# Kernel tuning notes

Hardware: AMD Instinct MI355X
Metric: run time of the kernel (lower is better)

The kernel has to match this reference:

```python
import jax, jax.numpy as jnp
import numpy as np

N = 50000          # nodes
E = 500000         # edges (before self-loops)
G = 64             # graphs in batch
SC = 96            # scalar features
D = 32             # embedding dim
IN_DIM = SC + 5 * D  # 256
C = 128            # hidden_channels
H1 = 4             # heads in conv1
NUM_CLASSES = 5
V_OP, V_SRC, V_SINK, V_STR, V_PAY = 256, 512, 512, 128, 1024


def setup_inputs() -> dict:
    key = jax.random.key(0)
    ks = jax.random.split(key, 32)
    inp = {}
    inp['x_scalar'] = jax.random.normal(ks[0], (N, SC), jnp.float32)
    inp['x_opcode'] = jax.random.randint(ks[1], (N, 16), 0, V_OP)
    inp['x_source'] = jax.random.randint(ks[2], (N, 8), 0, V_SRC)
    inp['x_sink'] = jax.random.randint(ks[3], (N, 8), 0, V_SINK)
    inp['x_string_manip'] = jax.random.randint(ks[4], (N, 8), 0, V_STR)
    inp['x_payload'] = jax.random.randint(ks[5], (N, 8), 0, V_PAY)
    inp['edge_index'] = jax.random.randint(ks[6], (2, E), 0, N)
    # sorted graph ids with every graph non-empty
    inp['batch'] = (jnp.arange(N) * G) // N
    # learned params
    s = 0.05
    inp['emb_opcode'] = jax.random.normal(ks[7], (V_OP, D), jnp.float32)
    inp['emb_source'] = jax.random.normal(ks[8], (V_SRC, D), jnp.float32)
    inp['emb_sink'] = jax.random.normal(ks[9], (V_SINK, D), jnp.float32)
    inp['emb_string'] = jax.random.normal(ks[10], (V_STR, D), jnp.float32)
    inp['emb_payload'] = jax.random.normal(ks[11], (V_PAY, D), jnp.float32)
    inp['ln_g'] = jnp.ones((IN_DIM,), jnp.float32)
    inp['ln_b'] = jnp.zeros((IN_DIM,), jnp.float32)
    inp['W1'] = jax.random.normal(ks[12], (IN_DIM, H1 * C), jnp.float32) * s
    inp['att_src1'] = jax.random.normal(ks[13], (H1, C), jnp.float32) * s
    inp['att_dst1'] = jax.random.normal(ks[14], (H1, C), jnp.float32) * s
    inp['b1'] = jnp.zeros((H1 * C,), jnp.float32)
    inp['W2'] = jax.random.normal(ks[15], (H1 * C, C), jnp.float32) * s
    inp['att_src2'] = jax.random.normal(ks[16], (1, C), jnp.float32) * s
    inp['att_dst2'] = jax.random.normal(ks[17], (1, C), jnp.float32) * s
    inp['b2'] = jnp.zeros((C,), jnp.float32)
    inp['Wc1'] = jax.random.normal(ks[18], (C, C // 2), jnp.float32) * s
    inp['bc1'] = jnp.zeros((C // 2,), jnp.float32)
    inp['Wc2'] = jax.random.normal(ks[19], (C // 2, NUM_CLASSES), jnp.float32) * s
    inp['bc2'] = jnp.zeros((NUM_CLASSES,), jnp.float32)
    return inp


def _emb_feat(table, idx):
    # masked mean over the list dim; index 0 is padding
    e = table[idx]                                  # [N, L, D]
    mask = (idx != 0)[..., None].astype(e.dtype)    # [N, L, 1]
    return (e * mask).sum(1) / (mask.sum(1) + 1e-9)


def _layernorm(x, g, b, eps=1e-5):
    mu = x.mean(-1, keepdims=True)
    var = ((x - mu) ** 2).mean(-1, keepdims=True)
    return (x - mu) * jax.lax.rsqrt(var + eps) * g + b


def _gat_conv(x, W, att_src, att_dst, bias, src, dst, heads, out_ch, concat):
    n = x.shape[0]
    h = (x @ W).reshape(n, heads, out_ch)              # [N,H,C]
    a_src = (h * att_src).sum(-1)                      # [N,H]
    a_dst = (h * att_dst).sum(-1)                      # [N,H]
    e = jax.nn.leaky_relu(a_src[src] + a_dst[dst], 0.2)  # [E,H]
    m = jax.ops.segment_max(e, dst, num_segments=n)
    e = jnp.exp(e - m[dst])
    denom = jax.ops.segment_sum(e, dst, num_segments=n)
    alpha = e / (denom[dst] + 1e-16)                   # segment softmax over in-edges
    msg = h[src] * alpha[:, :, None]                   # [E,H,C]
    out = jax.ops.segment_sum(msg, dst, num_segments=n)  # [N,H,C]
    out = out.reshape(n, heads * out_ch) if concat else out.mean(1)
    return out + bias


def reference(x_scalar, x_opcode, x_source, x_sink, x_string_manip, x_payload,
              edge_index, batch,
              emb_opcode, emb_source, emb_sink, emb_string, emb_payload,
              ln_g, ln_b, W1, att_src1, att_dst1, b1,
              W2, att_src2, att_dst2, b2, Wc1, bc1, Wc2, bc2):
    n = x_scalar.shape[0]
    feats = jnp.concatenate([
        x_scalar,
        _emb_feat(emb_opcode, x_opcode),
        _emb_feat(emb_source, x_source),
        _emb_feat(emb_sink, x_sink),
        _emb_feat(emb_string, x_string_manip),
        _emb_feat(emb_payload, x_payload),
    ], axis=1)
    feats = _layernorm(feats, ln_g, ln_b)
    # add self loops (PyG GATConv default)
    loop = jnp.arange(n)
    src = jnp.concatenate([edge_index[0], loop])
    dst = jnp.concatenate([edge_index[1], loop])
    x = jax.nn.elu(_gat_conv(feats, W1, att_src1, att_dst1, b1, src, dst, H1, C, True))
    x = jax.nn.elu(_gat_conv(x, W2, att_src2, att_dst2, b2, src, dst, 1, C, True))
    # global max pool per graph (dropout layers are identity at inference)
    xp = jax.ops.segment_max(x, batch, num_segments=G)  # [G,C]
    hcls = jax.nn.relu(xp @ Wc1 + bc1)
    return hcls @ Wc2 + bc2
```

## Files before the change

### kernel.cpp

```cpp
#include <hip/hip_runtime.h>
#include <hip/hip_bf16.h>
#include <float.h>


#define LEAKY(e) ((e) > 0.f ? (e) : 0.2f * (e))
#define POOL_CH 32

typedef _Float16 half8 __attribute__((ext_vector_type(8)));
typedef float floatx4 __attribute__((ext_vector_type(4)));

__device__ __forceinline__ void async_copy16(const _Float16* gsrc,
                                             const _Float16* ldst) {
  __builtin_amdgcn_global_load_lds(
      (const __attribute__((address_space(1))) unsigned int*)gsrc,
      (__attribute__((address_space(3))) unsigned int*)ldst, 16, 0, 0);
}

__global__ __launch_bounds__(256) void feats_kernel(
    const float* __restrict__ xs, const int* __restrict__ xo,
    const int* __restrict__ xsrc, const int* __restrict__ xsk,
    const int* __restrict__ xst, const int* __restrict__ xp,
    const float* __restrict__ eo, const float* __restrict__ es,
    const float* __restrict__ ek, const float* __restrict__ et,
    const float* __restrict__ ep, const float* __restrict__ lng,
    const float* __restrict__ lnb, _Float16* __restrict__ feats, int n) {
  int node = blockIdx.x * 4 + (threadIdx.x >> 6);
  if (node >= n) return;
  int l = threadIdx.x & 63;

  int myidx = 0;
  if (l < 16)      myidx = xo[node * 16 + l];
  else if (l < 24) myidx = xsrc[node * 8 + (l - 16)];
  else if (l < 32) myidx = xsk[node * 8 + (l - 24)];
  else if (l < 40) myidx = xst[node * 8 + (l - 32)];
  else if (l < 48) myidx = xp[node * 8 + (l - 40)];

  const float* xrow = xs + (size_t)node * 96;
  float v0 = xrow[l];
  float v1, v2, v3;

  bool hi = (l >= 32);
  int d = l & 31;

  {
    float s = 0.f, c = 0.f;
#pragma unroll
    for (int j = 0; j < 16; j++) {
      int id = __shfl(myidx, j);
      if (hi && id != 0) { s += eo[(size_t)id * 32 + d]; c += 1.f; }
    }
    float sc = hi ? 0.f : xrow[64 + l];
    v1 = hi ? (s / (c + 1e-9f)) : sc;
  }
  {
    const float* tab = hi ? ek : es;
    int base = hi ? 24 : 16;
    float s = 0.f, c = 0.f;
#pragma unroll
    for (int j = 0; j < 8; j++) {
      int id = __shfl(myidx, base + j);
      if (id != 0) { s += tab[(size_t)id * 32 + d]; c += 1.f; }
    }
    v2 = s / (c + 1e-9f);
  }
  {
    const float* tab = hi ? ep : et;
    int base = hi ? 40 : 32;
    float s = 0.f, c = 0.f;
#pragma unroll
    for (int j = 0; j < 8; j++) {
      int id = __shfl(myidx, base + j);
      if (id != 0) { s += tab[(size_t)id * 32 + d]; c += 1.f; }
    }
    v3 = s / (c + 1e-9f);
  }

  float sum = v0 + v1 + v2 + v3;
  for (int o = 32; o; o >>= 1) sum += __shfl_xor(sum, o);
  float mu = sum * (1.f / 256.f);

  float d0 = v0 - mu, d1 = v1 - mu, d2 = v2 - mu, d3 = v3 - mu;
  float q = d0 * d0 + d1 * d1 + d2 * d2 + d3 * d3;
  for (int o = 32; o; o >>= 1) q += __shfl_xor(q, o);
  float rstd = rsqrtf(q * (1.f / 256.f) + 1e-5f);

  _Float16* frow = feats + (size_t)node * 256;
  frow[l]       = (_Float16)(d0 * rstd * lng[l] + lnb[l]);
  frow[64 + l]  = (_Float16)(d1 * rstd * lng[64 + l] + lnb[64 + l]);
  frow[128 + l] = (_Float16)(d2 * rstd * lng[128 + l] + lnb[128 + l]);
  frow[192 + l] = (_Float16)(d3 * rstd * lng[192 + l] + lnb[192 + l]);
}

__global__ __launch_bounds__(256) void transpose_both_f16(
    const float* __restrict__ W1, _Float16* __restrict__ Wt1,
    const float* __restrict__ W2, _Float16* __restrict__ Wt2) {
  int t = blockIdx.x * 256 + threadIdx.x;
  if (t < 256 * 512) {
    int n = t / 256, k = t - n * 256;
    Wt1[t] = (_Float16)W1[(size_t)k * 512 + n];
  } else {
    int u = t - 256 * 512;
    int n = u / 512, k = u - n * 512;
    Wt2[u] = (_Float16)W2[(size_t)k * 128 + n];
  }
}

__global__ __launch_bounds__(256) void gemm_f16_att(
    const _Float16* __restrict__ A, const _Float16* __restrict__ Bt,
    _Float16* __restrict__ C, const float* __restrict__ att_src,
    const float* __restrict__ att_dst, float* __restrict__ a_src_out,
    float* __restrict__ a_dst_out, int astride, int K, int N) {
  __shared__ __attribute__((aligned(16))) _Float16 As[128 * 32];
  __shared__ __attribute__((aligned(16))) _Float16 Bs[128 * 32];
  int m0 = blockIdx.y * 128;
  int n0 = blockIdx.x * 128;
  int tid = threadIdx.x;
  int wave = tid >> 6, lane = tid & 63;
  int wm = (wave >> 1) * 64, wn = (wave & 1) * 64;
  int lr = lane & 15, lq = lane >> 4;
  int wbase = tid & ~63;

  floatx4 acc[4][4] = {};

  for (int k0 = 0; k0 < K; k0 += 32) {
#pragma unroll
    for (int c = 0; c < 2; c++) {
      int sid = c * 256 + tid;
      int row = sid >> 2;
      int cs = (sid & 3) ^ (row & 3);
      const _Float16* ga = A + (size_t)(m0 + row) * K + k0 + cs * 8;
      const _Float16* gb = Bt + (size_t)(n0 + row) * K + k0 + cs * 8;
      async_copy16(ga, As + (size_t)(c * 256 + wbase) * 8);
      async_copy16(gb, Bs + (size_t)(c * 256 + wbase) * 8);
    }
    __syncthreads();

    half8 af[4], bf[4];
#pragma unroll
    for (int i = 0; i < 4; i++) {
      int row = wm + i * 16 + lr;
      af[i] = *(const half8*)(As + ((row << 2) + (lq ^ (row & 3))) * 8);
    }
#pragma unroll
    for (int j = 0; j < 4; j++) {
      int row = wn + j * 16 + lr;
      bf[j] = *(const half8*)(Bs + ((row << 2) + (lq ^ (row & 3))) * 8);
    }
#pragma unroll
    for (int i = 0; i < 4; i++)
#pragma unroll
      for (int j = 0; j < 4; j++)
        acc[i][j] =
            __builtin_amdgcn_mfma_f32_16x16x32_f16(af[i], bf[j], acc[i][j], 0, 0, 0);
    __syncthreads();
  }

#pragma unroll
  for (int i = 0; i < 4; i++) {
    int rbase = m0 + wm + i * 16 + lq * 4;
#pragma unroll
    for (int r = 0; r < 4; r++) {
      int row = rbase + r;
#pragma unroll
      for (int j = 0; j < 4; j++) {
        int col = n0 + wn + j * 16 + lr;
        C[(size_t)row * N + col] = (_Float16)acc[i][j][r];
      }
    }
  }

  float asv[4], adv[4];
#pragma unroll
  for (int j = 0; j < 4; j++) {
    int col = n0 + wn + j * 16 + lr;
    asv[j] = att_src[col];
    adv[j] = att_dst[col];
  }
  float ps[4][4], pd[4][4];
#pragma unroll
  for (int i = 0; i < 4; i++)
#pragma unroll
    for (int r = 0; r < 4; r++) {
      float s = 0.f, d = 0.f;
#pragma unroll
      for (int j = 0; j < 4; j++) {
        s += acc[i][j][r] * asv[j];
        d += acc[i][j][r] * adv[j];
      }
#pragma unroll
      for (int o = 1; o < 16; o <<= 1) {
        s += __shfl_xor(s, o);
        d += __shfl_xor(d, o);
      }
      ps[i][r] = s;
      pd[i][r] = d;
    }
  float* sred = (float*)&As[0];
  if (wn == 64 && lr == 0) {
#pragma unroll
    for (int i = 0; i < 4; i++)
#pragma unroll
      for (int r = 0; r < 4; r++) {
        int rl = wm + i * 16 + lq * 4 + r;
        sred[rl * 2] = ps[i][r];
        sred[rl * 2 + 1] = pd[i][r];
      }
  }
  __syncthreads();
  if (wn == 0 && lr == 0) {
    int hsel = n0 >> 7;
#pragma unroll
    for (int i = 0; i < 4; i++)
#pragma unroll
      for (int r = 0; r < 4; r++) {
        int rl = wm + i * 16 + lq * 4 + r;
        int row = m0 + rl;
        a_src_out[(size_t)row * astride + hsel] = ps[i][r] + sred[rl * 2];
        a_dst_out[(size_t)row * astride + hsel] = pd[i][r] + sred[rl * 2 + 1];
      }
  }
}

__global__ __launch_bounds__(256) void hist_kernel(const int* __restrict__ dst,
                                                   int* __restrict__ deg, int E) {
  int t = blockIdx.x * 256 + threadIdx.x;
  if (t < E) atomicAdd(&deg[dst[t]], 1);
}

__global__ __launch_bounds__(256) void scan_a(const int* __restrict__ deg,
                                              int* __restrict__ rowptr,
                                              int* __restrict__ bsum, int n) {
  __shared__ int sh[256];
  int b = blockIdx.x, t = threadIdx.x;
  int i = b * 256 + t;
  int v = (i < n) ? deg[i] + 1 : 0;
  sh[t] = v;
  __syncthreads();
  int x = v;
  for (int o = 1; o < 256; o <<= 1) {
    int y = (t >= o) ? sh[t - o] : 0;
    __syncthreads();
    x += y;
    sh[t] = x;
    __syncthreads();
  }
  if (i < n) rowptr[i] = x - v;
  if (t == 255) bsum[b] = x;
}

__global__ __launch_bounds__(256) void scan_c(int* __restrict__ rowptr,
                                              const int* __restrict__ bsum,
                                              int n, int total) {
  int b = blockIdx.x;
  int off = 0;
  for (int j = 0; j < b; j++) off += bsum[j];
  int i = b * 256 + threadIdx.x;
  if (i < n) rowptr[i] += off;
  else if (i == n) rowptr[n] = total;
}

__global__ __launch_bounds__(256) void fill_kernel(
    const int* __restrict__ src, const int* __restrict__ dst,
    const int* __restrict__ rowptr, int* __restrict__ cnt,
    int* __restrict__ csr_src, int E, int n) {
  int t = blockIdx.x * 256 + threadIdx.x;
  if (t < E) {
    int d = dst[t];
    int pos = rowptr[d] + atomicAdd(&cnt[d], 1);
    csr_src[pos] = src[t];
  } else if (t < E + n) {
    int i = t - E;
    csr_src[rowptr[i + 1] - 1] = i;
  }
}

__global__ __launch_bounds__(256) void gat1_agg(
    const _Float16* __restrict__ h1, const float* __restrict__ asrc,
    const float* __restrict__ adst, const int* __restrict__ rowptr,
    const int* __restrict__ csr_src, const float* __restrict__ bias,
    _Float16* __restrict__ out, int n) {
  int node = blockIdx.x * 4 + (threadIdx.x >> 6);
  if (node >= n) return;
  int l = threadIdx.x & 63;
  int hh = l >> 4;
  int li = l & 15;
  int r0 = rowptr[node];
  int deg = rowptr[node + 1] - r0;
  int cb = l * 8;

  float acc[8] = {};

  if (deg <= 64) {
    float adm = adst[node * 4 + hh];
    int s_reg[4];
    float ww[4];
    float m = -1e30f;
#pragma unroll
    for (int c = 0; c < 4; c++) {
      int k = c * 16 + li;
      int s = (k < deg) ? csr_src[r0 + k] : -1;
      s_reg[c] = s;
      float e = -1e30f;
      if (s >= 0) {
        float t = asrc[(size_t)s * 4 + hh] + adm;
        e = LEAKY(t);
      }
      ww[c] = e;
      m = fmaxf(m, e);
    }
#pragma unroll
    for (int o = 1; o < 16; o <<= 1) m = fmaxf(m, __shfl_xor(m, o));
    float sum = 0.f;
#pragma unroll
    for (int c = 0; c < 4; c++) {
      float w = (s_reg[c] >= 0) ? __expf(ww[c] - m) : 0.f;
      ww[c] = w;
      sum += w;
    }
#pragma unroll
    for (int o = 1; o < 16; o <<= 1) sum += __shfl_xor(sum, o);
    float sinv = 1.f / (sum + 1e-16f);
#pragma unroll
    for (int c = 0; c < 4; c++) ww[c] *= sinv;

#pragma unroll
    for (int c = 0; c < 4; c++) {
      int base = c * 16;
      if (base >= deg) break;
      int lim = min(16, deg - base);
      int jl = 0;
      for (; jl + 4 <= lim; jl += 4) {
        int s0 = __shfl(s_reg[c], jl);
        int s1 = __shfl(s_reg[c], jl + 1);
        int s2 = __shfl(s_reg[c], jl + 2);
        int s3 = __shfl(s_reg[c], jl + 3);
        float w0 = __shfl(ww[c], hh * 16 + jl);
        float w1 = __shfl(ww[c], hh * 16 + jl + 1);
        float w2 = __shfl(ww[c], hh * 16 + jl + 2);
        float w3 = __shfl(ww[c], hh * 16 + jl + 3);
        const half8 hv0 = *(const half8*)(h1 + (size_t)s0 * 512 + cb);
        const half8 hv1 = *(const half8*)(h1 + (size_t)s1 * 512 + cb);
        const half8 hv2 = *(const half8*)(h1 + (size_t)s2 * 512 + cb);
        const half8 hv3 = *(const half8*)(h1 + (size_t)s3 * 512 + cb);
#pragma unroll
        for (int q = 0; q < 8; q++)
          acc[q] += w0 * (float)hv0[q] + w1 * (float)hv1[q] +
                    w2 * (float)hv2[q] + w3 * (float)hv3[q];
      }
      for (; jl < lim; jl++) {
        int s0 = __shfl(s_reg[c], jl);
        float w0 = __shfl(ww[c], hh * 16 + jl);
        const half8 hv0 = *(const half8*)(h1 + (size_t)s0 * 512 + cb);
#pragma unroll
        for (int q = 0; q < 8; q++) acc[q] += w0 * (float)hv0[q];
      }
    }
  } else {
    float4 ad4 = *(const float4*)(adst + node * 4);
    float adv[4] = {ad4.x, ad4.y, ad4.z, ad4.w};
    float m[4] = {-1e30f, -1e30f, -1e30f, -1e30f};
    for (int k = l; k < deg; k += 64) {
      int s = csr_src[r0 + k];
      float4 av = *(const float4*)(asrc + (size_t)s * 4);
      float e;
      e = LEAKY(av.x + adv[0]); m[0] = fmaxf(m[0], e);
      e = LEAKY(av.y + adv[1]); m[1] = fmaxf(m[1], e);
      e = LEAKY(av.z + adv[2]); m[2] = fmaxf(m[2], e);
      e = LEAKY(av.w + adv[3]); m[3] = fmaxf(m[3], e);
    }
    for (int o = 1; o < 64; o <<= 1) {
#pragma unroll
      for (int h = 0; h < 4; h++) m[h] = fmaxf(m[h], __shfl_xor(m[h], o));
    }
    float sum[4] = {0.f, 0.f, 0.f, 0.f};
    for (int k = l; k < deg; k += 64) {
      int s = csr_src[r0 + k];
      float4 av = *(const float4*)(asrc + (size_t)s * 4);
      float e;
      e = LEAKY(av.x + adv[0]); sum[0] += __expf(e - m[0]);
      e = LEAKY(av.y + adv[1]); sum[1] += __expf(e - m[1]);
      e = LEAKY(av.z + adv[2]); sum[2] += __expf(e - m[2]);
      e = LEAKY(av.w + adv[3]); sum[3] += __expf(e - m[3]);
    }
    for (int o = 1; o < 64; o <<= 1) {
#pragma unroll
      for (int h = 0; h < 4; h++) sum[h] += __shfl_xor(sum[h], o);
    }
    float mm = m[hh];
    float sinv = 1.f / (sum[hh] + 1e-16f);
    float adm = adv[hh];
    for (int k = 0; k < deg; k++) {
      int s = csr_src[r0 + k];
      float a = asrc[(size_t)s * 4 + hh];
      float e = LEAKY(a + adm);
      float w = __expf(e - mm) * sinv;
      const half8 hv = *(const half8*)(h1 + (size_t)s * 512 + cb);
#pragma unroll
      for (int q = 0; q < 8; q++) acc[q] += w * (float)hv[q];
    }
  }

  const float* bp = bias + cb;
  half8 ov;
#pragma unroll
  for (int j = 0; j < 8; j++) {
    float r = acc[j] + bp[j];
    ov[j] = (_Float16)(r > 0.f ? r : (__expf(r) - 1.f));
  }
  *(half8*)(out + (size_t)node * 512 + cb) = ov;
}

__global__ __launch_bounds__(256) void gat2_agg(
    const _Float16* __restrict__ h2, const float* __restrict__ asrc,
    const float* __restrict__ adst, const int* __restrict__ rowptr,
    const int* __restrict__ csr_src, const float* __restrict__ bias,
    _Float16* __restrict__ out, int n) {
  int node = blockIdx.x * 4 + (threadIdx.x >> 6);
  if (node >= n) return;
  int l = threadIdx.x & 63;
  int r0 = rowptr[node];
  int deg = rowptr[node + 1] - r0;

  if (deg <= 64) {
    float ad = adst[node];
    int s = (l < deg) ? csr_src[r0 + l] : -1;
    float e = -1e30f;
    if (s >= 0) {
      float t = asrc[s] + ad;
      e = LEAKY(t);
    }
    float m = e;
    for (int o = 1; o < 64; o <<= 1) m = fmaxf(m, __shfl_xor(m, o));
    float w = (s >= 0) ? __expf(e - m) : 0.f;
    float sum = w;
    for (int o = 1; o < 64; o <<= 1) sum += __shfl_xor(sum, o);
    w *= 1.f / (sum + 1e-16f);

    int g4 = l >> 4;
    int ch = (l & 15) * 8;
    float acc[8] = {};
    for (int j = 0; j < deg; j += 4) {
      int je = j + g4;
      int jc = min(je, 63);
      int sj = __shfl(s, jc);
      float wj = (je < deg) ? __shfl(w, jc) : 0.f;
      if (sj < 0) sj = 0;
      const half8 hv = *(const half8*)(h2 + (size_t)sj * 128 + ch);
#pragma unroll
      for (int q = 0; q < 8; q++) acc[q] += wj * (float)hv[q];
    }
#pragma unroll
    for (int q = 0; q < 8; q++) {
      acc[q] += __shfl_xor(acc[q], 16);
      acc[q] += __shfl_xor(acc[q], 32);
    }
    if (l < 16) {
      half8 ov;
#pragma unroll
      for (int q = 0; q < 8; q++) {
        float r = acc[q] + bias[ch + q];
        ov[q] = (_Float16)(r > 0.f ? r : (__expf(r) - 1.f));
      }
      *(half8*)(out + (size_t)node * 128 + ch) = ov;
    }
  } else {
    float ad = adst[node];
    float m = -1e30f;
    for (int k = l; k < deg; k += 64) {
      int s = csr_src[r0 + k];
      float e = LEAKY(asrc[s] + ad);
      m = fmaxf(m, e);
    }
    for (int o = 1; o < 64; o <<= 1) m = fmaxf(m, __shfl_xor(m, o));
    float sum = 0.f;
    for (int k = l; k < deg; k += 64) {
      int s = csr_src[r0 + k];
      float e = LEAKY(asrc[s] + ad);
      sum += __expf(e - m);
    }
    for (int o = 1; o < 64; o <<= 1) sum += __shfl_xor(sum, o);
    float sinv = 1.f / (sum + 1e-16f);
    int cb = l * 2;
    float a0 = 0.f, a1 = 0.f;
    for (int k = 0; k < deg; k++) {
      int s = csr_src[r0 + k];
      float e = LEAKY(asrc[s] + ad);
      float w = __expf(e - m) * sinv;
      const _Float16* hp = h2 + (size_t)s * 128 + cb;
      a0 += w * (float)hp[0];
      a1 += w * (float)hp[1];
    }
    float ra = a0 + bias[cb];
    float rb = a1 + bias[cb + 1];
    out[(size_t)node * 128 + cb]     = (_Float16)(ra > 0.f ? ra : (__expf(ra) - 1.f));
    out[(size_t)node * 128 + cb + 1] = (_Float16)(rb > 0.f ? rb : (__expf(rb) - 1.f));
  }
}

__device__ inline int lower_bound_i(const int* a, int n, int v) {
  int lo = 0, hi = n;
  while (lo < hi) {
    int mid = (lo + hi) >> 1;
    if (a[mid] < v) lo = mid + 1; else hi = mid;
  }
  return lo;
}

__global__ __launch_bounds__(128) void pool_partial(
    const _Float16* __restrict__ x2, const int* __restrict__ batch,
    float* __restrict__ partial, int n) {
  int g = blockIdx.y;
  int j = blockIdx.x;
  int t = threadIdx.x;
  int start = lower_bound_i(batch, n, g);
  int end = lower_bound_i(batch, n, g + 1);
  int len = end - start;
  int c0 = start + (int)((long long)len * j / POOL_CH);
  int c1 = start + (int)((long long)len * (j + 1) / POOL_CH);
  float m = -FLT_MAX;
  for (int i = c0; i < c1; i++) m = fmaxf(m, (float)x2[(size_t)i * 128 + t]);
  partial[((size_t)g * POOL_CH + j) * 128 + t] = m;
}

__global__ __launch_bounds__(128) void pool_final(
    const float* __restrict__ partial, float* __restrict__ pool) {
  int g = blockIdx.x;
  int t = threadIdx.x;
  float m = -FLT_MAX;
#pragma unroll
  for (int j = 0; j < POOL_CH; j++)
    m = fmaxf(m, partial[((size_t)g * POOL_CH + j) * 128 + t]);
  pool[g * 128 + t] = m;
}

__global__ __launch_bounds__(64) void classifier_kernel(
    const float* __restrict__ pool, const float* __restrict__ Wc1,
    const float* __restrict__ bc1, const float* __restrict__ Wc2,
    const float* __restrict__ bc2, float* __restrict__ out) {
  int g = blockIdx.x;
  int t = threadIdx.x;
  __shared__ float xp[128];
  __shared__ float hc[64];
  xp[t] = pool[g * 128 + t];
  xp[t + 64] = pool[g * 128 + 64 + t];
  __syncthreads();
  float s = bc1[t];
  for (int k = 0; k < 128; k++) s += xp[k] * Wc1[k * 64 + t];
  hc[t] = s > 0.f ? s : 0.f;
  __syncthreads();
  if (t < 5) {
    float o = bc2[t];
    for (int j = 0; j < 64; j++) o += hc[j] * Wc2[j * 5 + t];
    out[g * 5 + t] = o;
  }
}

extern "C" void kernel_launch(void* const* d_in, const int* in_sizes, int n_in,
                              void* d_out, int out_size, void* d_ws, size_t ws_size,
                              hipStream_t stream) {
  const float* x_scalar = (const float*)d_in[0];
  const int* x_opcode = (const int*)d_in[1];
  const int* x_source = (const int*)d_in[2];
  const int* x_sink = (const int*)d_in[3];
  const int* x_string = (const int*)d_in[4];
  const int* x_payload = (const int*)d_in[5];
  const int* edge_index = (const int*)d_in[6];
  const int* batch = (const int*)d_in[7];
  const float* emb_opcode = (const float*)d_in[8];
  const float* emb_source = (const float*)d_in[9];
  const float* emb_sink = (const float*)d_in[10];
  const float* emb_string = (const float*)d_in[11];
  const float* emb_payload = (const float*)d_in[12];
  const float* ln_g = (const float*)d_in[13];
  const float* ln_b = (const float*)d_in[14];
  const float* W1 = (const float*)d_in[15];
  const float* att_src1 = (const float*)d_in[16];
  const float* att_dst1 = (const float*)d_in[17];
  const float* b1 = (const float*)d_in[18];
  const float* W2 = (const float*)d_in[19];
  const float* att_src2 = (const float*)d_in[20];
  const float* att_dst2 = (const float*)d_in[21];
  const float* b2 = (const float*)d_in[22];
  const float* Wc1 = (const float*)d_in[23];
  const float* bc1 = (const float*)d_in[24];
  const float* Wc2 = (const float*)d_in[25];
  const float* bc2 = (const float*)d_in[26];
  float* out = (float*)d_out;

  const int N = in_sizes[0] / 96;
  const int E = in_sizes[6] / 2;
  const int G = out_size / 5;
  const int Npad = (N + 127) / 128 * 128;

  const int* e_src = edge_index;
  const int* e_dst = edge_index + E;

  char* w = (char*)d_ws;
  size_t o = 0;
  auto take = [&](size_t bytes) -> void* {
    void* p = w + o;
    o += (bytes + 255) & ~(size_t)255;
    return p;
  };
  char* regionA = (char*)take((size_t)Npad * 256 * 2);
  char* regionB = (char*)take((size_t)Npad * 512 * 2);
  _Float16* x1 = (_Float16*)take((size_t)Npad * 512 * 2);
  _Float16* Wt1 = (_Float16*)take((size_t)512 * 256 * 2);
  _Float16* Wt2 = (_Float16*)take((size_t)128 * 512 * 2);
  float* a_src1 = (float*)take((size_t)Npad * 4 * 4);
  float* a_dst1 = (float*)take((size_t)Npad * 4 * 4);
  float* a_src2 = (float*)take((size_t)Npad * 4);
  float* a_dst2 = (float*)take((size_t)Npad * 4);
  int* deg = (int*)take((size_t)N * 2 * 4);
  int* cnt = deg + N;
  int* rowptr = (int*)take((size_t)(N + 1) * 4);
  int* csr_src = (int*)take((size_t)(E + N) * 4);
  int* bsum = (int*)take(256 * 4);

  _Float16* feats = (_Float16*)regionA;
  _Float16* h2 = (_Float16*)regionA;
  float* partial = (float*)(regionA + (((size_t)Npad * 128 * 2 + 255) & ~(size_t)255));
  float* pool = partial + (size_t)G * POOL_CH * 128;
  _Float16* h1 = (_Float16*)regionB;
  _Float16* x2 = (_Float16*)regionB;

  hipMemsetAsync(deg, 0, (size_t)N * 2 * 4, stream);

  hist_kernel<<<(E + 255) / 256, 256, 0, stream>>>(e_dst, deg, E);
  int nb = (N + 255) / 256;
  scan_a<<<nb, 256, 0, stream>>>(deg, rowptr, bsum, N);
  scan_c<<<(N + 256) / 256, 256, 0, stream>>>(rowptr, bsum, N, E + N);
  fill_kernel<<<(E + N + 255) / 256, 256, 0, stream>>>(e_src, e_dst, rowptr, cnt,
                                                       csr_src, E, N);

  transpose_both_f16<<<(256 * 512 + 512 * 128 + 255) / 256, 256, 0, stream>>>(
      W1, Wt1, W2, Wt2);

  feats_kernel<<<(N + 3) / 4, 256, 0, stream>>>(
      x_scalar, x_opcode, x_source, x_sink, x_string, x_payload, emb_opcode,
      emb_source, emb_sink, emb_string, emb_payload, ln_g, ln_b, feats, N);

  int mblocks = Npad / 128;
  gemm_f16_att<<<dim3(512 / 128, mblocks), 256, 0, stream>>>(
      feats, Wt1, h1, att_src1, att_dst1, a_src1, a_dst1, 4, 256, 512);
  gat1_agg<<<(N + 3) / 4, 256, 0, stream>>>(h1, a_src1, a_dst1, rowptr, csr_src,
                                            b1, x1, N);

  gemm_f16_att<<<dim3(128 / 128, mblocks), 256, 0, stream>>>(
      x1, Wt2, h2, att_src2, att_dst2, a_src2, a_dst2, 1, 512, 128);
  gat2_agg<<<(N + 3) / 4, 256, 0, stream>>>(h2, a_src2, a_dst2, rowptr, csr_src,
                                            b2, x2, N);

  pool_partial<<<dim3(POOL_CH, G), 128, 0, stream>>>(x2, batch, partial, N);
  pool_final<<<G, 128, 0, stream>>>(partial, pool);
  classifier_kernel<<<G, 64, 0, stream>>>(pool, Wc1, bc1, Wc2, bc2, out);
}
```

Before: 440.4 us.

## Fuse setup kernels, single-block scan, and fold max-pool into GAT2 aggregation

Merges the degree histogram, weight transpose and feature/LayerNorm kernels into one launch that splits work by block range. The two-pass multi-block scan becomes a single 1024-thread block scan that also writes a working copy of rowptr, so the fill step no longer needs a separate counter array. Global max pooling now happens inside the second GAT aggregation through atomicMax on order-preserving float keys, which removes the x2 write and the two pool kernels. The cost is atomic contention on 64x128 pool slots and a serial per-thread chunk loop in the single-block scan.

```diff
diff --git a/kernel.cpp b/kernel.cpp
--- a/kernel.cpp
+++ b/kernel.cpp
@@ -4,7 +4,6 @@
 
 
 #define LEAKY(e) ((e) > 0.f ? (e) : 0.2f * (e))
-#define POOL_CH 32
 
 typedef _Float16 half8 __attribute__((ext_vector_type(8)));
 typedef float floatx4 __attribute__((ext_vector_type(4)));
@@ -16,7 +15,18 @@
       (__attribute__((address_space(3))) unsigned int*)ldst, 16, 0, 0);
 }
 
-__global__ __launch_bounds__(256) void feats_kernel(
+__device__ __forceinline__ unsigned fkey(float f) {
+  unsigned b = __float_as_uint(f);
+  return (b & 0x80000000u) ? ~b : (b | 0x80000000u);
+}
+__device__ __forceinline__ float fdec(unsigned k) {
+  return __uint_as_float((k & 0x80000000u) ? (k & 0x7FFFFFFFu) : ~k);
+}
+
+__global__ __launch_bounds__(256) void setup_kernel(
+    const int* __restrict__ e_dst, int* __restrict__ deg, int E, int HB,
+    const float* __restrict__ W1, _Float16* __restrict__ Wt1,
+    const float* __restrict__ W2, _Float16* __restrict__ Wt2, int TB,
     const float* __restrict__ xs, const int* __restrict__ xo,
     const int* __restrict__ xsrc, const int* __restrict__ xsk,
     const int* __restrict__ xst, const int* __restrict__ xp,
@@ -24,7 +34,25 @@
     const float* __restrict__ ek, const float* __restrict__ et,
     const float* __restrict__ ep, const float* __restrict__ lng,
     const float* __restrict__ lnb, _Float16* __restrict__ feats, int n) {
-  int node = blockIdx.x * 4 + (threadIdx.x >> 6);
+  int b = blockIdx.x;
+  if (b < HB) {
+    int t = b * 256 + threadIdx.x;
+    if (t < E) atomicAdd(&deg[e_dst[t]], 1);
+    return;
+  }
+  if (b < HB + TB) {
+    int t = (b - HB) * 256 + threadIdx.x;
+    if (t < 256 * 512) {
+      int nn = t / 256, k = t - nn * 256;
+      Wt1[t] = (_Float16)W1[(size_t)k * 512 + nn];
+    } else {
+      int u = t - 256 * 512;
+      int nn = u / 512, k = u - nn * 512;
+      Wt2[u] = (_Float16)W2[(size_t)k * 128 + nn];
+    }
+    return;
+  }
+  int node = (b - HB - TB) * 4 + (threadIdx.x >> 6);
   if (node >= n) return;
   int l = threadIdx.x & 63;
 
@@ -38,10 +66,8 @@
   const float* xrow = xs + (size_t)node * 96;
   float v0 = xrow[l];
   float v1, v2, v3;
-
   bool hi = (l >= 32);
   int d = l & 31;
-
   {
     float s = 0.f, c = 0.f;
 #pragma unroll
@@ -78,7 +104,6 @@
   float sum = v0 + v1 + v2 + v3;
   for (int o = 32; o; o >>= 1) sum += __shfl_xor(sum, o);
   float mu = sum * (1.f / 256.f);
-
   float d0 = v0 - mu, d1 = v1 - mu, d2 = v2 - mu, d3 = v3 - mu;
   float q = d0 * d0 + d1 * d1 + d2 * d2 + d3 * d3;
   for (int o = 32; o; o >>= 1) q += __shfl_xor(q, o);
@@ -91,17 +116,45 @@
   frow[192 + l] = (_Float16)(d3 * rstd * lng[192 + l] + lnb[192 + l]);
 }
 
-__global__ __launch_bounds__(256) void transpose_both_f16(
-    const float* __restrict__ W1, _Float16* __restrict__ Wt1,
-    const float* __restrict__ W2, _Float16* __restrict__ Wt2) {
+__global__ __launch_bounds__(1024) void scan_kernel(
+    const int* __restrict__ deg, int* __restrict__ rowptr,
+    int* __restrict__ rowptr_work, int n) {
+  __shared__ int part[1024];
+  int t = threadIdx.x;
+  int chunk = (n + 1023) / 1024;
+  int s = t * chunk;
+  int e = min(s + chunk, n);
+  int sum = 0;
+  for (int i = s; i < e; i++) sum += deg[i] + 1;
+  part[t] = sum;
+  __syncthreads();
+  for (int off = 1; off < 1024; off <<= 1) {
+    int v = (t >= off) ? part[t - off] : 0;
+    __syncthreads();
+    part[t] += v;
+    __syncthreads();
+  }
+  int run = part[t] - sum;
+  for (int i = s; i < e; i++) {
+    rowptr[i] = run;
+    rowptr_work[i] = run;
+    run += deg[i] + 1;
+  }
+  if (e == n && s < n) rowptr[n] = run;
+}
+
+__global__ __launch_bounds__(256) void fill_kernel(
+    const int* __restrict__ src, const int* __restrict__ dst,
+    const int* __restrict__ rowptr, int* __restrict__ rowptr_work,
+    int* __restrict__ csr_src, int E, int n) {
   int t = blockIdx.x * 256 + threadIdx.x;
-  if (t < 256 * 512) {
-    int n = t / 256, k = t - n * 256;
-    Wt1[t] = (_Float16)W1[(size_t)k * 512 + n];
-  } else {
-    int u = t - 256 * 512;
-    int n = u / 512, k = u - n * 512;
-    Wt2[u] = (_Float16)W2[(size_t)k * 128 + n];
+  if (t < E) {
+    int d = dst[t];
+    int pos = atomicAdd(&rowptr_work[d], 1);
+    csr_src[pos] = src[t];
+  } else if (t < E + n) {
+    int i = t - E;
+    csr_src[rowptr[i + 1] - 1] = i;
   }
 }
 
@@ -218,59 +271,6 @@
         a_src_out[(size_t)row * astride + hsel] = ps[i][r] + sred[rl * 2];
         a_dst_out[(size_t)row * astride + hsel] = pd[i][r] + sred[rl * 2 + 1];
       }
-  }
-}
-
-__global__ __launch_bounds__(256) void hist_kernel(const int* __restrict__ dst,
-                                                   int* __restrict__ deg, int E) {
-  int t = blockIdx.x * 256 + threadIdx.x;
-  if (t < E) atomicAdd(&deg[dst[t]], 1);
-}
-
-__global__ __launch_bounds__(256) void scan_a(const int* __restrict__ deg,
-                                              int* __restrict__ rowptr,
-                                              int* __restrict__ bsum, int n) {
-  __shared__ int sh[256];
-  int b = blockIdx.x, t = threadIdx.x;
-  int i = b * 256 + t;
-  int v = (i < n) ? deg[i] + 1 : 0;
-  sh[t] = v;
-  __syncthreads();
-  int x = v;
-  for (int o = 1; o < 256; o <<= 1) {
-    int y = (t >= o) ? sh[t - o] : 0;
-    __syncthreads();
-    x += y;
-    sh[t] = x;
-    __syncthreads();
-  }
-  if (i < n) rowptr[i] = x - v;
-  if (t == 255) bsum[b] = x;
-}
-
-__global__ __launch_bounds__(256) void scan_c(int* __restrict__ rowptr,
-                                              const int* __restrict__ bsum,
-                                              int n, int total) {
-  int b = blockIdx.x;
-  int off = 0;
-  for (int j = 0; j < b; j++) off += bsum[j];
-  int i = b * 256 + threadIdx.x;
-  if (i < n) rowptr[i] += off;
-  else if (i == n) rowptr[n] = total;
-}
-
-__global__ __launch_bounds__(256) void fill_kernel(
-    const int* __restrict__ src, const int* __restrict__ dst,
-    const int* __restrict__ rowptr, int* __restrict__ cnt,
-    int* __restrict__ csr_src, int E, int n) {
-  int t = blockIdx.x * 256 + threadIdx.x;
-  if (t < E) {
-    int d = dst[t];
-    int pos = rowptr[d] + atomicAdd(&cnt[d], 1);
-    csr_src[pos] = src[t];
-  } else if (t < E + n) {
-    int i = t - E;
-    csr_src[rowptr[i + 1] - 1] = i;
   }
 }
 
@@ -410,16 +410,18 @@
   *(half8*)(out + (size_t)node * 512 + cb) = ov;
 }
 
-__global__ __launch_bounds__(256) void gat2_agg(
+__global__ __launch_bounds__(256) void gat2_agg_pool(
     const _Float16* __restrict__ h2, const float* __restrict__ asrc,
     const float* __restrict__ adst, const int* __restrict__ rowptr,
     const int* __restrict__ csr_src, const float* __restrict__ bias,
-    _Float16* __restrict__ out, int n) {
+    const int* __restrict__ batch, unsigned* __restrict__ poolkey, int n) {
   int node = blockIdx.x * 4 + (threadIdx.x >> 6);
   if (node >= n) return;
   int l = threadIdx.x & 63;
   int r0 = rowptr[node];
   int deg = rowptr[node + 1] - r0;
+  int g = batch[node];
+  unsigned* pk = poolkey + (size_t)g * 128;
 
   if (deg <= 64) {
     float ad = adst[node];
@@ -455,13 +457,12 @@
       acc[q] += __shfl_xor(acc[q], 32);
     }
     if (l < 16) {
-      half8 ov;
 #pragma unroll
       for (int q = 0; q < 8; q++) {
         float r = acc[q] + bias[ch + q];
-        ov[q] = (_Float16)(r > 0.f ? r : (__expf(r) - 1.f));
-      }
-      *(half8*)(out + (size_t)node * 128 + ch) = ov;
+        float v = r > 0.f ? r : (__expf(r) - 1.f);
+        atomicMax(&pk[ch + q], fkey(v));
+      }
     }
   } else {
     float ad = adst[node];
@@ -492,57 +493,23 @@
     }
     float ra = a0 + bias[cb];
     float rb = a1 + bias[cb + 1];
-    out[(size_t)node * 128 + cb]     = (_Float16)(ra > 0.f ? ra : (__expf(ra) - 1.f));
-    out[(size_t)node * 128 + cb + 1] = (_Float16)(rb > 0.f ? rb : (__expf(rb) - 1.f));
-  }
-}
-
-__device__ inline int lower_bound_i(const int* a, int n, int v) {
-  int lo = 0, hi = n;
-  while (lo < hi) {
-    int mid = (lo + hi) >> 1;
-    if (a[mid] < v) lo = mid + 1; else hi = mid;
-  }
-  return lo;
-}
-
-__global__ __launch_bounds__(128) void pool_partial(
-    const _Float16* __restrict__ x2, const int* __restrict__ batch,
-    float* __restrict__ partial, int n) {
-  int g = blockIdx.y;
-  int j = blockIdx.x;
-  int t = threadIdx.x;
-  int start = lower_bound_i(batch, n, g);
-  int end = lower_bound_i(batch, n, g + 1);
-  int len = end - start;
-  int c0 = start + (int)((long long)len * j / POOL_CH);
-  int c1 = start + (int)((long long)len * (j + 1) / POOL_CH);
-  float m = -FLT_MAX;
-  for (int i = c0; i < c1; i++) m = fmaxf(m, (float)x2[(size_t)i * 128 + t]);
-  partial[((size_t)g * POOL_CH + j) * 128 + t] = m;
-}
-
-__global__ __launch_bounds__(128) void pool_final(
-    const float* __restrict__ partial, float* __restrict__ pool) {
-  int g = blockIdx.x;
-  int t = threadIdx.x;
-  float m = -FLT_MAX;
-#pragma unroll
-  for (int j = 0; j < POOL_CH; j++)
-    m = fmaxf(m, partial[((size_t)g * POOL_CH + j) * 128 + t]);
-  pool[g * 128 + t] = m;
+    float va = ra > 0.f ? ra : (__expf(ra) - 1.f);
+    float vb = rb > 0.f ? rb : (__expf(rb) - 1.f);
+    atomicMax(&pk[cb], fkey(va));
+    atomicMax(&pk[cb + 1], fkey(vb));
+  }
 }
 
 __global__ __launch_bounds__(64) void classifier_kernel(
-    const float* __restrict__ pool, const float* __restrict__ Wc1,
+    const unsigned* __restrict__ poolkey, const float* __restrict__ Wc1,
     const float* __restrict__ bc1, const float* __restrict__ Wc2,
     const float* __restrict__ bc2, float* __restrict__ out) {
   int g = blockIdx.x;
   int t = threadIdx.x;
   __shared__ float xp[128];
   __shared__ float hc[64];
-  xp[t] = pool[g * 128 + t];
-  xp[t + 64] = pool[g * 128 + 64 + t];
+  xp[t] = fdec(poolkey[g * 128 + t]);
+  xp[t + 64] = fdec(poolkey[g * 128 + 64 + t]);
   __syncthreads();
   float s = bc1[t];
   for (int k = 0; k < 128; k++) s += xp[k] * Wc1[k * 64 + t];
@@ -611,47 +578,39 @@
   float* a_dst1 = (float*)take((size_t)Npad * 4 * 4);
   float* a_src2 = (float*)take((size_t)Npad * 4);
   float* a_dst2 = (float*)take((size_t)Npad * 4);
-  int* deg = (int*)take((size_t)N * 2 * 4);
-  int* cnt = deg + N;
+  int* deg = (int*)take((size_t)(N + G * 128) * 4);
+  unsigned* poolkey = (unsigned*)(deg + N);
   int* rowptr = (int*)take((size_t)(N + 1) * 4);
+  int* rowptr_work = (int*)take((size_t)N * 4);
   int* csr_src = (int*)take((size_t)(E + N) * 4);
-  int* bsum = (int*)take(256 * 4);
 
   _Float16* feats = (_Float16*)regionA;
   _Float16* h2 = (_Float16*)regionA;
-  float* partial = (float*)(regionA + (((size_t)Npad * 128 * 2 + 255) & ~(size_t)255));
-  float* pool = partial + (size_t)G * POOL_CH * 128;
   _Float16* h1 = (_Float16*)regionB;
-  _Float16* x2 = (_Float16*)regionB;
-
-  hipMemsetAsync(deg, 0, (size_t)N * 2 * 4, stream);
-
-  hist_kernel<<<(E + 255) / 256, 256, 0, stream>>>(e_dst, deg, E);
-  int nb = (N + 255) / 256;
-  scan_a<<<nb, 256, 0, stream>>>(deg, rowptr, bsum, N);
-  scan_c<<<(N + 256) / 256, 256, 0, stream>>>(rowptr, bsum, N, E + N);
-  fill_kernel<<<(E + N + 255) / 256, 256, 0, stream>>>(e_src, e_dst, rowptr, cnt,
-                                                       csr_src, E, N);
-
-  transpose_both_f16<<<(256 * 512 + 512 * 128 + 255) / 256, 256, 0, stream>>>(
-      W1, Wt1, W2, Wt2);
-
-  feats_kernel<<<(N + 3) / 4, 256, 0, stream>>>(
-      x_scalar, x_opcode, x_source, x_sink, x_string, x_payload, emb_opcode,
-      emb_source, emb_sink, emb_string, emb_payload, ln_g, ln_b, feats, N);
+
+  hipMemsetAsync(deg, 0, (size_t)(N + G * 128) * 4, stream);
+
+  int HB = (E + 255) / 256;
+  int TB = (256 * 512 + 512 * 128 + 255) / 256;
+  int FB = (N + 3) / 4;
+  setup_kernel<<<HB + TB + FB, 256, 0, stream>>>(
+      e_dst, deg, E, HB, W1, Wt1, W2, Wt2, TB, x_scalar, x_opcode, x_source,
+      x_sink, x_string, x_payload, emb_opcode, emb_source, emb_sink, emb_string,
+      emb_payload, ln_g, ln_b, feats, N);
+
+  scan_kernel<<<1, 1024, 0, stream>>>(deg, rowptr, rowptr_work, N);
+
+  fill_kernel<<<(E + N + 255) / 256, 256, 0, stream>>>(e_src, e_dst, rowptr,
+                                                       rowptr_work, csr_src, E, N);
 
   int mblocks = Npad / 128;
   gemm_f16_att<<<dim3(512 / 128, mblocks), 256, 0, stream>>>(
       feats, Wt1, h1, att_src1, att_dst1, a_src1, a_dst1, 4, 256, 512);
   gat1_agg<<<(N + 3) / 4, 256, 0, stream>>>(h1, a_src1, a_dst1, rowptr, csr_src,
                                             b1, x1, N);
-
   gemm_f16_att<<<dim3(128 / 128, mblocks), 256, 0, stream>>>(
       x1, Wt2, h2, att_src2, att_dst2, a_src2, a_dst2, 1, 512, 128);
-  gat2_agg<<<(N + 3) / 4, 256, 0, stream>>>(h2, a_src2, a_dst2, rowptr, csr_src,
-                                            b2, x2, N);
-
-  pool_partial<<<dim3(POOL_CH, G), 128, 0, stream>>>(x2, batch, partial, N);
-  pool_final<<<G, 128, 0, stream>>>(partial, pool);
-  classifier_kernel<<<G, 64, 0, stream>>>(pool, Wc1, bc1, Wc2, bc2, out);
-}
+  gat2_agg_pool<<<(N + 3) / 4, 256, 0, stream>>>(h2, a_src2, a_dst2, rowptr,
+                                                 csr_src, b2, batch, poolkey, N);
+  classifier_kernel<<<G, 64, 0, stream>>>(poolkey, Wc1, bc1, Wc2, bc2, out);
+}
```

New measurement: 863.8 us. 1.96x slower.
